# Kernel optimization log

Measured on AMD Instinct MI355X. Metric: run time of the kernel, lower is better.

The kernel has to match this reference:

```python
import jax, jax.numpy as jnp
import numpy as np
from jax import lax

C = 128
HEADS = 8
HID = 256  # int(C * 2.0)
B, H, W = 8, 128, 128
EPS_LN = 1e-5
EPS_NORM = 1e-12


def _dwconv(x, w, pad):
    # x: [B,C,H,W], w: [C,1,kh,kw] depthwise
    return lax.conv_general_dilated(
        x, w, window_strides=(1, 1), padding=[(pad, pad), (pad, pad)],
        dimension_numbers=("NCHW", "OIHW", "NCHW"), feature_group_count=x.shape[1])


def _conv1x1(x, w):
    # w: [O, I] pointwise conv
    return jnp.einsum("oi,bihw->bohw", w, x)


def _layernorm_c(x, gamma, beta):
    # torch: reshape to [B, HW, C], LayerNorm over C, reshape back == LN over channel axis
    mu = jnp.mean(x, axis=1, keepdims=True)
    var = jnp.mean(jnp.square(x - mu), axis=1, keepdims=True)
    xn = (x - mu) * lax.rsqrt(var + EPS_LN)
    return xn * gamma[None, :, None, None] + beta[None, :, None, None]


def _l2norm(x):
    n = jnp.sqrt(jnp.sum(jnp.square(x), axis=-1, keepdims=True))
    return x / jnp.maximum(n, EPS_NORM)


def _mdta(x, qkv_w, qkv_dw, temperature, attn_proj):
    b, c, h, w = x.shape
    qkv = _dwconv(_conv1x1(x, qkv_w), qkv_dw, pad=1)  # [B,3C,H,W]
    q, k, v = jnp.split(qkv, 3, axis=1)
    hd = c // HEADS
    q = q.reshape(b, HEADS, hd, h * w)
    k = k.reshape(b, HEADS, hd, h * w)
    v = v.reshape(b, HEADS, hd, h * w)
    q, k = _l2norm(q), _l2norm(k)
    attn = jax.nn.softmax(jnp.einsum("bhdn,bhen->bhde", q, k) * temperature, axis=-1)
    out = jnp.einsum("bhde,bhen->bhdn", attn, v).reshape(b, c, h, w)
    return _conv1x1(out, attn_proj)


def _gdfn2(x, pin_w, c1_w, c3_w, c5_w, pout_w):
    x = _conv1x1(x, pin_w)  # [B,HID,H,W]
    x1 = x * c1_w[None, :, 0, 0, 0, None, None]  # depthwise 1x1 == per-channel scale
    x3 = _dwconv(x, c3_w, pad=1)
    x5 = _dwconv(x, c5_w, pad=2)
    g = jax.nn.gelu(x1, approximate=False)
    gated = jnp.concatenate([g * x3, g * x5], axis=1)  # [B,2*HID,H,W]
    return _conv1x1(gated, pout_w)


def setup_inputs() -> dict:
    key = jax.random.key(0)
    ks = jax.random.split(key, 12)
    s = 0.05
    return {
        "x": jax.random.normal(ks[0], (B, C, H, W), jnp.float32),
        "ln1_w": jnp.ones((C,), jnp.float32),
        "ln1_b": jnp.zeros((C,), jnp.float32),
        "qkv_w": jax.random.normal(ks[1], (3 * C, C), jnp.float32) * s,
        "qkv_dw": jax.random.normal(ks[2], (3 * C, 1, 3, 3), jnp.float32) * s,
        "temperature": jnp.ones((1, HEADS, 1, 1), jnp.float32),
        "attn_proj": jax.random.normal(ks[3], (C, C), jnp.float32) * s,
        "ln2_w": jnp.ones((C,), jnp.float32),
        "ln2_b": jnp.zeros((C,), jnp.float32),
        "pin_w": jax.random.normal(ks[4], (HID, C), jnp.float32) * s,
        "c1_w": jax.random.normal(ks[5], (HID, 1, 1, 1), jnp.float32) * s,
        "c3_w": jax.random.normal(ks[6], (HID, 1, 3, 3), jnp.float32) * s,
        "c5_w": jax.random.normal(ks[7], (HID, 1, 5, 5), jnp.float32) * s,
        "pout_w": jax.random.normal(ks[8], (C, 2 * HID), jnp.float32) * s,
    }


def reference(x, ln1_w, ln1_b, qkv_w, qkv_dw, temperature, attn_proj,
              ln2_w, ln2_b, pin_w, c1_w, c3_w, c5_w, pout_w):
    x = x + _mdta(_layernorm_c(x, ln1_w, ln1_b), qkv_w, qkv_dw, temperature, attn_proj)
    x = x + _gdfn2(_layernorm_c(x, ln2_w, ln2_b), pin_w, c1_w, c3_w, c5_w, pout_w)
    return x
```

## Files before the change

kernel.cpp:

```cpp
#include <hip/hip_runtime.h>
#include <type_traits>

typedef unsigned short ushort;
typedef unsigned int uint;
typedef __bf16 bf16x8 __attribute__((ext_vector_type(8)));
typedef unsigned short ushort8v __attribute__((ext_vector_type(8)));
typedef float f32x4 __attribute__((ext_vector_type(4)));

__device__ __forceinline__ float b2f(ushort u) {
    unsigned int x = ((unsigned int)u) << 16;
    float f;
    __builtin_memcpy(&f, &x, 4);
    return f;
}
__device__ __forceinline__ ushort f2bf(float f) {
    unsigned int x;
    __builtin_memcpy(&x, &f, 4);
    unsigned int r = x + 0x7fffu + ((x >> 16) & 1u);
    return (ushort)(r >> 16);
}
__device__ __forceinline__ float u2f_lo(uint u) {
    uint x = u << 16;
    float f;
    __builtin_memcpy(&f, &x, 4);
    return f;
}
__device__ __forceinline__ float u2f_hi(uint u) {
    uint x = u & 0xffff0000u;
    float f;
    __builtin_memcpy(&f, &x, 4);
    return f;
}
__device__ __forceinline__ uint packbf(float a, float b) {
    return (uint)f2bf(a) | ((uint)f2bf(b) << 16);
}

#define NPIX 16384
#define PSTRIDE 136

__device__ __forceinline__ size_t tadr(int b, int CH, int tile, int ch, int off) {
    return (((size_t)b * 256 + tile) * CH + ch) * 64 + off;
}
__device__ __forceinline__ size_t padr(int b, int tile, int p, int c) {
    return (((size_t)b * 256 + tile) * 64 + p) * 128 + c;
}

__device__ __forceinline__ void stage_plane(ushort* pl, const ushort* __restrict__ src,
                                            int b, int c, int CH, int tid) {
    uint* plu = (uint*)pl;
    for (int i = tid; i < 784; i += 256) {
        int idx;
        if (i < 136) idx = i;
        else if (i < 272) idx = 8840 + (i - 136);
        else {
            int j = i - 272;
            int r = (j >> 2) + 2;
            int cs = j & 3;
            idx = r * 68 + (cs == 0 ? 0 : 64 + cs);
        }
        plu[idx] = 0u;
    }
    for (int i = tid; i < 2048; i += 256) {
        int row = i >> 4, xg = (i & 15) << 3;
        int px0 = row * 128 + xg;
        uint4 v = *(const uint4*)&src[tadr(b, CH, px0 >> 6, c, px0 & 63)];
        uint* dst = (uint*)&pl[(row + 2) * PSTRIDE + xg + 2];
        dst[0] = v.x; dst[1] = v.y; dst[2] = v.z; dst[3] = v.w;
    }
    __syncthreads();
}

__device__ __forceinline__ void unpack12(const ushort* rowp, float* cc) {
    const uint* rp = (const uint*)rowp;
    uint4 u = *(const uint4*)rp;
    uint2 v = *(const uint2*)(rp + 4);
    cc[0] = u2f_lo(u.x); cc[1] = u2f_hi(u.x);
    cc[2] = u2f_lo(u.y); cc[3] = u2f_hi(u.y);
    cc[4] = u2f_lo(u.z); cc[5] = u2f_hi(u.z);
    cc[6] = u2f_lo(u.w); cc[7] = u2f_hi(u.w);
    cc[8] = u2f_lo(v.x); cc[9] = u2f_hi(v.x);
    cc[10] = u2f_lo(v.y); cc[11] = u2f_hi(v.y);
}

__global__ __launch_bounds__(256) void wcvt(const float* __restrict__ s0, ushort* __restrict__ d0, int n0,
                                            const float* __restrict__ s1, ushort* __restrict__ d1, int n1,
                                            const float* __restrict__ s2, ushort* __restrict__ d2, int n2) {
    int i = blockIdx.x * 256 + threadIdx.x;
    if (i < n0) d0[i] = f2bf(s0[i]);
    else if (i < n0 + n1) d1[i - n0] = f2bf(s1[i - n0]);
    else if (i < n0 + n1 + n2) d2[i - n0 - n1] = f2bf(s2[i - n0 - n1]);
}

template <int O>
__global__ __launch_bounds__(256) void ln_gemm_mfma(const float* __restrict__ xin,
                                                    const ushort* __restrict__ Wb,
                                                    const float* __restrict__ gamma,
                                                    const float* __restrict__ beta,
                                                    ushort* __restrict__ out) {
    __shared__ ushort xs[64][136];
    __shared__ float red[2][4][64];
    __shared__ float mu[64], rs[64];
    __shared__ float gl[128], bl[128];

    const int blk = blockIdx.x;
    const int b = blk >> 8;
    const int tile = blk & 255;
    const int tid = threadIdx.x;

    const float* xb = xin + (size_t)b * 128 * NPIX + tile * 64;
    float vx[4][8];
#pragma unroll
    for (int k = 0; k < 4; k++) {
        int i = tid + k * 256;
        int p = i & 63, cg = i >> 6;
        const float* src = xb + (size_t)(cg * 8) * NPIX + p;
#pragma unroll
        for (int j = 0; j < 8; j++) vx[k][j] = src[(size_t)j * NPIX];
    }
    if (tid < 128) {
        gl[tid] = gamma[tid];
        bl[tid] = beta[tid];
    }
#pragma unroll
    for (int k = 0; k < 4; k++) {
        int i = tid + k * 256;
        int p = i & 63, cg = i >> 6;
        ushort8v u;
#pragma unroll
        for (int j = 0; j < 8; j++) u[j] = f2bf(vx[k][j]);
        *(ushort8v*)&xs[p][cg * 8] = u;
    }
    __syncthreads();

    {
        const int p = tid & 63, part = tid >> 6;
        float s = 0.f, ss = 0.f;
#pragma unroll
        for (int q = 0; q < 4; q++) {
            ushort8v u = *(const ushort8v*)&xs[p][part * 32 + q * 8];
#pragma unroll
            for (int j = 0; j < 8; j++) {
                float v = b2f(u[j]);
                s += v;
                ss += v * v;
            }
        }
        red[0][part][p] = s;
        red[1][part][p] = ss;
    }
    __syncthreads();
    if (tid < 64) {
        float s = red[0][0][tid] + red[0][1][tid] + red[0][2][tid] + red[0][3][tid];
        float ss = red[1][0][tid] + red[1][1][tid] + red[1][2][tid] + red[1][3][tid];
        float m = s * (1.f / 128.f);
        float var = ss * (1.f / 128.f) - m * m;
        mu[tid] = m;
        rs[tid] = rsqrtf(var + 1e-5f);
    }
    __syncthreads();
    {
        const int p = tid & 63, part = tid >> 6;
        const float mp = mu[p], rp = rs[p];
#pragma unroll
        for (int q = 0; q < 4; q++) {
            int c0 = part * 32 + q * 8;
            ushort8v u = *(const ushort8v*)&xs[p][c0];
            ushort8v o;
#pragma unroll
            for (int j = 0; j < 8; j++) {
                float v = b2f(u[j]);
                o[j] = f2bf((v - mp) * rp * gl[c0 + j] + bl[c0 + j]);
            }
            *(ushort8v*)&xs[p][c0] = o;
        }
    }
    __syncthreads();

    const int wv = tid >> 6, lane = tid & 63;
    const int lr = lane & 15, lg = lane >> 4;

    bf16x8 bfr[4][4];
#pragma unroll
    for (int t = 0; t < 4; t++)
#pragma unroll
        for (int kc = 0; kc < 4; kc++)
            bfr[t][kc] = __builtin_bit_cast(bf16x8, *(const ushort8v*)&xs[t * 16 + lr][kc * 32 + lg * 8]);

    constexpr int MT = O / 64;
#pragma unroll 1
    for (int mt = 0; mt < MT; mt++) {
        const int o0 = (wv * MT + mt) * 16;
        bf16x8 afr[4];
#pragma unroll
        for (int kc = 0; kc < 4; kc++)
            afr[kc] = __builtin_bit_cast(bf16x8,
                *(const ushort8v*)&Wb[(size_t)(o0 + lr) * 128 + kc * 32 + lg * 8]);
        f32x4 acc[4] = {{0.f, 0.f, 0.f, 0.f}, {0.f, 0.f, 0.f, 0.f}, {0.f, 0.f, 0.f, 0.f}, {0.f, 0.f, 0.f, 0.f}};
#pragma unroll
        for (int kc = 0; kc < 4; kc++)
#pragma unroll
            for (int t = 0; t < 4; t++)
                acc[t] = __builtin_amdgcn_mfma_f32_16x16x32_bf16(afr[kc], bfr[t][kc], acc[t], 0, 0, 0);
#pragma unroll
        for (int t = 0; t < 4; t++)
#pragma unroll
            for (int r = 0; r < 4; r++) {
                int o = o0 + lg * 4 + r;
                out[tadr(b, O, tile, o, t * 16 + lr)] = f2bf(acc[t][r]);
            }
    }
}

__global__ __launch_bounds__(256) void dwconv3_lds(const ushort* __restrict__ in,
                                                   const float* __restrict__ wdw,
                                                   ushort* __restrict__ out, int CH) {
    __shared__ ushort pl[132 * PSTRIDE];
    const int c = blockIdx.x;
    const int b = blockIdx.y;
    const int tid = threadIdx.x;

    float w[9];
#pragma unroll
    for (int j = 0; j < 9; j++) w[j] = wdw[c * 9 + j];

    stage_plane(pl, in, b, c, CH, tid);

    const int x = (tid & 15) * 8;
    const int ybase = tid >> 4;
#pragma unroll 1
    for (int k = 0; k < 8; k++) {
        const int y = k * 16 + ybase;
        float a[8];
#pragma unroll
        for (int p = 0; p < 8; p++) a[p] = 0.f;
#pragma unroll
        for (int ky = 0; ky < 3; ky++) {
            float cc[12];
            unpack12(&pl[(y + ky + 1) * PSTRIDE + x], cc);
#pragma unroll
            for (int kx = 0; kx < 3; kx++) {
                float wv = w[ky * 3 + kx];
#pragma unroll
                for (int p = 0; p < 8; p++) a[p] += cc[p + kx + 1] * wv;
            }
        }
        const int px0 = (y << 7) + x;
        uint4 o;
        o.x = packbf(a[0], a[1]);
        o.y = packbf(a[2], a[3]);
        o.z = packbf(a[4], a[5]);
        o.w = packbf(a[6], a[7]);
        *(uint4*)&out[tadr(b, CH, px0 >> 6, c, px0 & 63)] = o;
    }
}

__global__ __launch_bounds__(256) void dw_gated(const ushort* __restrict__ t,
                                                const float* __restrict__ w3_,
                                                const float* __restrict__ w5_,
                                                const float* __restrict__ c1w,
                                                ushort* __restrict__ gated) {
    __shared__ ushort pl[132 * PSTRIDE];
    const int c = blockIdx.x;
    const int b = blockIdx.y;
    const int tid = threadIdx.x;

    float w3[9], w5[25];
#pragma unroll
    for (int j = 0; j < 9; j++) w3[j] = w3_[c * 9 + j];
#pragma unroll
    for (int j = 0; j < 25; j++) w5[j] = w5_[c * 25 + j];
    const float c1v = c1w[c];

    stage_plane(pl, t, b, c, 256, tid);

    const int x = (tid & 15) * 8;
    const int ybase = tid >> 4;
#pragma unroll 1
    for (int k = 0; k < 8; k++) {
        const int y = k * 16 + ybase;
        float a5[8], a3[8], tc[8];
#pragma unroll
        for (int p = 0; p < 8; p++) { a5[p] = 0.f; a3[p] = 0.f; }
#pragma unroll
        for (int ky = 0; ky < 5; ky++) {
            float cc[12];
            unpack12(&pl[(y + ky) * PSTRIDE + x], cc);
#pragma unroll
            for (int kx = 0; kx < 5; kx++) {
                float wv = w5[ky * 5 + kx];
#pragma unroll
                for (int p = 0; p < 8; p++) a5[p] += cc[p + kx] * wv;
            }
            if (ky >= 1 && ky <= 3) {
#pragma unroll
                for (int kx = 0; kx < 3; kx++) {
                    float wv = w3[(ky - 1) * 3 + kx];
#pragma unroll
                    for (int p = 0; p < 8; p++) a3[p] += cc[p + kx + 1] * wv;
                }
            }
            if (ky == 2) {
#pragma unroll
                for (int p = 0; p < 8; p++) tc[p] = cc[p + 2];
            }
        }
        const int px0 = (y << 7) + x;
        uint4 o3, o5;
        float g[8];
#pragma unroll
        for (int p = 0; p < 8; p++) {
            float x1 = tc[p] * c1v;
            g[p] = x1 * __builtin_amdgcn_rcpf(1.f + __expf(-1.702f * x1));
        }
        o3.x = packbf(g[0] * a3[0], g[1] * a3[1]);
        o3.y = packbf(g[2] * a3[2], g[3] * a3[3]);
        o3.z = packbf(g[4] * a3[4], g[5] * a3[5]);
        o3.w = packbf(g[6] * a3[6], g[7] * a3[7]);
        o5.x = packbf(g[0] * a5[0], g[1] * a5[1]);
        o5.y = packbf(g[2] * a5[2], g[3] * a5[3]);
        o5.z = packbf(g[4] * a5[4], g[5] * a5[5]);
        o5.w = packbf(g[6] * a5[6], g[7] * a5[7]);
        *(uint4*)&gated[tadr(b, 512, px0 >> 6, c, px0 & 63)] = o3;
        *(uint4*)&gated[tadr(b, 512, px0 >> 6, 256 + c, px0 & 63)] = o5;
    }
}

__global__ __launch_bounds__(256) void attn_M(const ushort* __restrict__ qkv,
                                              const float* __restrict__ temp,
                                              const float* __restrict__ attn_proj,
                                              ushort* __restrict__ M) {
    __shared__ float Sp[4][16][16];
    __shared__ float QSS[4][16], KSS[4][16];
    __shared__ float A[16][17];

    const int bh = blockIdx.x, b = bh >> 3, h = bh & 7;
    const int tid = threadIdx.x;
    const int w = tid >> 6, lane = tid & 63;
    const int lr = lane & 15, lg = lane >> 4;

    const size_t qbase = (((size_t)b * 256 + w * 64) * 384 + h * 16 + lr) * 64 + lg * 8;
    const size_t kbase = qbase + (size_t)128 * 64;

    f32x4 acc = {0.f, 0.f, 0.f, 0.f};
    f32x4 accq = {0.f, 0.f, 0.f, 0.f};
    f32x4 acck = {0.f, 0.f, 0.f, 0.f};
#pragma unroll 2
    for (int it = 0; it < 128; it++) {
        size_t off = (size_t)(it >> 1) * (384 * 64) + (it & 1) * 32;
        bf16x8 qf = __builtin_bit_cast(bf16x8, *(const ushort8v*)(qkv + qbase + off));
        bf16x8 kf = __builtin_bit_cast(bf16x8, *(const ushort8v*)(qkv + kbase + off));
        acc = __builtin_amdgcn_mfma_f32_16x16x32_bf16(qf, kf, acc, 0, 0, 0);
        accq = __builtin_amdgcn_mfma_f32_16x16x32_bf16(qf, qf, accq, 0, 0, 0);
        acck = __builtin_amdgcn_mfma_f32_16x16x32_bf16(kf, kf, acck, 0, 0, 0);
    }
#pragma unroll
    for (int r = 0; r < 4; r++) Sp[w][lg * 4 + r][lr] = acc[r];
    if (lg == (lr >> 2)) {
        QSS[w][lr] = accq[lr & 3];
        KSS[w][lr] = acck[lr & 3];
    }
    __syncthreads();

    const int d = tid >> 4, e = tid & 15;
    float S = Sp[0][d][e] + Sp[1][d][e] + Sp[2][d][e] + Sp[3][d][e];
    float nq = fmaxf(sqrtf(QSS[0][d] + QSS[1][d] + QSS[2][d] + QSS[3][d]), 1e-12f);
    float nk = fmaxf(sqrtf(KSS[0][e] + KSS[1][e] + KSS[2][e] + KSS[3][e]), 1e-12f);
    float logit = S / (nq * nk) * temp[h];
    float m = logit;
    for (int off = 8; off; off >>= 1) m = fmaxf(m, __shfl_xor(m, off, 64));
    float ex = expf(logit - m);
    float sum = ex;
    for (int off = 8; off; off >>= 1) sum += __shfl_xor(sum, off, 64);
    A[d][e] = ex / sum;
    __syncthreads();

    for (int i = tid; i < 2048; i += 256) {
        int o = i >> 4, ee = i & 15;
        float acc2 = 0.f;
#pragma unroll
        for (int dd = 0; dd < 16; dd++) acc2 += attn_proj[o * 128 + h * 16 + dd] * A[dd][ee];
        M[((size_t)b * 128 + o) * 128 + h * 16 + ee] = f2bf(acc2);
    }
}

__global__ __launch_bounds__(256) void mv_ln_mfma(const ushort* __restrict__ qkv,
                                                  const ushort* __restrict__ Mb16,
                                                  const float* __restrict__ x,
                                                  const ushort* __restrict__ pin_b,
                                                  const float* __restrict__ gamma,
                                                  const float* __restrict__ beta,
                                                  ushort* __restrict__ x2,
                                                  ushort* __restrict__ t_out) {
    __shared__ ushort vs[64][136];
    __shared__ ushort xs[64][136];
    __shared__ float red[2][4][64];
    __shared__ float mu[64], rs[64];
    __shared__ float gl[128], bl[128];

    const int blk = blockIdx.x;
    const int b = blk >> 8;
    const int tile = blk & 255;
    const int tid = threadIdx.x;
    const int wv = tid >> 6, lane = tid & 63;
    const int lr = lane & 15, lg = lane >> 4;

    const ushort* vb = qkv + tadr(b, 384, tile, 256, 0);
    ushort8v vv[4];
#pragma unroll
    for (int k = 0; k < 4; k++) {
        int idx = tid + k * 256;
        int c = idx & 127, pg = idx >> 7;
        vv[k] = *(const ushort8v*)&vb[c * 64 + pg * 8];
    }
    if (tid < 128) {
        gl[tid] = gamma[tid];
        bl[tid] = beta[tid];
    }
#pragma unroll
    for (int k = 0; k < 4; k++) {
        int idx = tid + k * 256;
        int c = idx & 127, pg = idx >> 7;
#pragma unroll
        for (int j = 0; j < 8; j++) vs[pg * 8 + j][c] = vv[k][j];
    }
    __syncthreads();

    bf16x8 bfr[4][4];
#pragma unroll
    for (int t = 0; t < 4; t++)
#pragma unroll
        for (int kc = 0; kc < 4; kc++)
            bfr[t][kc] = __builtin_bit_cast(bf16x8, *(const ushort8v*)&vs[t * 16 + lr][kc * 32 + lg * 8]);

    const ushort* Mb = Mb16 + (size_t)b * 128 * 128;
#pragma unroll 1
    for (int mt = 0; mt < 2; mt++) {
        const int o0 = (wv * 2 + mt) * 16;
        bf16x8 afr[4];
#pragma unroll
        for (int kc = 0; kc < 4; kc++)
            afr[kc] = __builtin_bit_cast(bf16x8,
                *(const ushort8v*)&Mb[(size_t)(o0 + lr) * 128 + kc * 32 + lg * 8]);
        f32x4 acc[4] = {{0.f, 0.f, 0.f, 0.f}, {0.f, 0.f, 0.f, 0.f}, {0.f, 0.f, 0.f, 0.f}, {0.f, 0.f, 0.f, 0.f}};
#pragma unroll
        for (int kc = 0; kc < 4; kc++)
#pragma unroll
            for (int t = 0; t < 4; t++)
                acc[t] = __builtin_amdgcn_mfma_f32_16x16x32_bf16(afr[kc], bfr[t][kc], acc[t], 0, 0, 0);
#pragma unroll
        for (int t = 0; t < 4; t++) {
            int px = t * 16 + lr;
            const float* xp = &x[((size_t)b * 128 + o0 + lg * 4) * NPIX + tile * 64 + px];
            uint2 pk;
            pk.x = packbf(xp[0] + acc[t][0], xp[NPIX] + acc[t][1]);
            pk.y = packbf(xp[2 * NPIX] + acc[t][2], xp[3 * NPIX] + acc[t][3]);
            *(uint2*)&xs[px][o0 + lg * 4] = pk;
        }
    }
    __syncthreads();

#pragma unroll
    for (int k = 0; k < 4; k++) {
        int idx = tid + k * 256;
        int p = idx >> 4, seg = idx & 15;
        uint4 v = *(const uint4*)&xs[p][seg * 8];
        *(uint4*)&x2[padr(b, tile, p, seg * 8)] = v;
    }
    {
        const int p = tid & 63, part = tid >> 6;
        float s = 0.f, ss = 0.f;
#pragma unroll
        for (int q = 0; q < 4; q++) {
            ushort8v u = *(const ushort8v*)&xs[p][part * 32 + q * 8];
#pragma unroll
            for (int j = 0; j < 8; j++) {
                float v = b2f(u[j]);
                s += v;
                ss += v * v;
            }
        }
        red[0][part][p] = s;
        red[1][part][p] = ss;
    }
    __syncthreads();
    if (tid < 64) {
        float s = red[0][0][tid] + red[0][1][tid] + red[0][2][tid] + red[0][3][tid];
        float ss = red[1][0][tid] + red[1][1][tid] + red[1][2][tid] + red[1][3][tid];
        float m = s * (1.f / 128.f);
        float var = ss * (1.f / 128.f) - m * m;
        mu[tid] = m;
        rs[tid] = rsqrtf(var + 1e-5f);
    }
    __syncthreads();
    {
        const int p = tid & 63, part = tid >> 6;
        const float mp = mu[p], rp = rs[p];
#pragma unroll
        for (int q = 0; q < 4; q++) {
            int c0 = part * 32 + q * 8;
            ushort8v u = *(const ushort8v*)&xs[p][c0];
            ushort8v o;
#pragma unroll
            for (int j = 0; j < 8; j++) {
                float v = b2f(u[j]);
                o[j] = f2bf((v - mp) * rp * gl[c0 + j] + bl[c0 + j]);
            }
            *(ushort8v*)&xs[p][c0] = o;
        }
    }
    __syncthreads();

    bf16x8 bfr2[4][4];
#pragma unroll
    for (int t = 0; t < 4; t++)
#pragma unroll
        for (int kc = 0; kc < 4; kc++)
            bfr2[t][kc] = __builtin_bit_cast(bf16x8, *(const ushort8v*)&xs[t * 16 + lr][kc * 32 + lg * 8]);

#pragma unroll 1
    for (int mt = 0; mt < 4; mt++) {
        const int o0 = (wv * 4 + mt) * 16;
        bf16x8 afr[4];
#pragma unroll
        for (int kc = 0; kc < 4; kc++)
            afr[kc] = __builtin_bit_cast(bf16x8,
                *(const ushort8v*)&pin_b[(size_t)(o0 + lr) * 128 + kc * 32 + lg * 8]);
        f32x4 acc[4] = {{0.f, 0.f, 0.f, 0.f}, {0.f, 0.f, 0.f, 0.f}, {0.f, 0.f, 0.f, 0.f}, {0.f, 0.f, 0.f, 0.f}};
#pragma unroll
        for (int kc = 0; kc < 4; kc++)
#pragma unroll
            for (int t = 0; t < 4; t++)
                acc[t] = __builtin_amdgcn_mfma_f32_16x16x32_bf16(afr[kc], bfr2[t][kc], acc[t], 0, 0, 0);
#pragma unroll
        for (int t = 0; t < 4; t++)
#pragma unroll
            for (int r = 0; r < 4; r++) {
                int o = o0 + lg * 4 + r;
                t_out[tadr(b, 256, tile, o, t * 16 + lr)] = f2bf(acc[t][r]);
            }
    }
}

__global__ __launch_bounds__(256) void gdfn_mfma(const ushort* __restrict__ gated,
                                                 const ushort* __restrict__ x2,
                                                 const ushort* __restrict__ pout_b,
                                                 float* __restrict__ out) {
    __shared__ ushort gs[2][64][72];

    const int blk = blockIdx.x;
    const int b = blk >> 8;
    const int tile = blk & 255;
    const int tid = threadIdx.x;
    const int wv = tid >> 6, lane = tid & 63;
    const int lr = lane & 15, lg = lane >> 4;

    const ushort* gb = gated + tadr(b, 512, tile, 0, 0);
    const int c0 = tid & 63;
    const int pg0 = tid >> 6;

    ushort8v pa[8], pb[8];
#pragma unroll
    for (int k = 0; k < 8; k++) {
        const ushort* nb = gb + k * 4096;
        pa[k] = *(const ushort8v*)&nb[c0 * 64 + pg0 * 8];
        pb[k] = *(const ushort8v*)&nb[c0 * 64 + (pg0 + 4) * 8];
    }

    f32x4 acc[2][4];
#pragma unroll
    for (int mt = 0; mt < 2; mt++)
#pragma unroll
        for (int tt = 0; tt < 4; tt++) acc[mt][tt] = (f32x4){0.f, 0.f, 0.f, 0.f};

#pragma unroll
    for (int j = 0; j < 8; j++) {
        gs[0][pg0 * 8 + j][c0] = pa[0][j];
        gs[0][(pg0 + 4) * 8 + j][c0] = pb[0][j];
    }
    __syncthreads();

#pragma unroll
    for (int kb = 0; kb < 8; kb++) {
        const int cur = kb & 1;

        bf16x8 bfrg[4][2];
#pragma unroll
        for (int tt = 0; tt < 4; tt++)
#pragma unroll
            for (int kc = 0; kc < 2; kc++)
                bfrg[tt][kc] = __builtin_bit_cast(bf16x8, *(const ushort8v*)&gs[cur][tt * 16 + lr][kc * 32 + lg * 8]);

#pragma unroll
        for (int mt = 0; mt < 2; mt++) {
            const int o0 = (wv * 2 + mt) * 16;
            bf16x8 afr[2];
#pragma unroll
            for (int kc = 0; kc < 2; kc++)
                afr[kc] = __builtin_bit_cast(bf16x8,
                    *(const ushort8v*)&pout_b[(size_t)(o0 + lr) * 512 + kb * 64 + kc * 32 + lg * 8]);
#pragma unroll
            for (int kc = 0; kc < 2; kc++)
#pragma unroll
                for (int tt = 0; tt < 4; tt++)
                    acc[mt][tt] = __builtin_amdgcn_mfma_f32_16x16x32_bf16(afr[kc], bfrg[tt][kc], acc[mt][tt], 0, 0, 0);
        }

        if (kb < 7) {
#pragma unroll
            for (int j = 0; j < 8; j++) {
                gs[cur ^ 1][pg0 * 8 + j][c0] = pa[kb + 1][j];
                gs[cur ^ 1][(pg0 + 4) * 8 + j][c0] = pb[kb + 1][j];
            }
        }
        __syncthreads();
    }

#pragma unroll
    for (int mt = 0; mt < 2; mt++)
#pragma unroll
        for (int tt = 0; tt < 4; tt++) {
            int o0 = (wv * 2 + mt) * 16 + lg * 4;
            int px = tt * 16 + lr;
            uint2 xw = *(const uint2*)&x2[padr(b, tile, px, o0)];
            float xv0 = u2f_lo(xw.x), xv1 = u2f_hi(xw.x);
            float xv2 = u2f_lo(xw.y), xv3 = u2f_hi(xw.y);
            size_t obase = ((size_t)b * 128 + o0) * NPIX + tile * 64 + px;
            out[obase] = xv0 + acc[mt][tt][0];
            out[obase + NPIX] = xv1 + acc[mt][tt][1];
            out[obase + 2 * NPIX] = xv2 + acc[mt][tt][2];
            out[obase + 3 * NPIX] = xv3 + acc[mt][tt][3];
        }
}

extern "C" void kernel_launch(void* const* d_in, const int* in_sizes, int n_in,
                              void* d_out, int out_size, void* d_ws, size_t ws_size,
                              hipStream_t stream) {
    const float* x = (const float*)d_in[0];
    const float* ln1_w = (const float*)d_in[1];
    const float* ln1_b = (const float*)d_in[2];
    const float* qkv_w = (const float*)d_in[3];
    const float* qkv_dw = (const float*)d_in[4];
    const float* temperature = (const float*)d_in[5];
    const float* attn_proj = (const float*)d_in[6];
    const float* ln2_w = (const float*)d_in[7];
    const float* ln2_b = (const float*)d_in[8];
    const float* pin_w = (const float*)d_in[9];
    const float* c1_w = (const float*)d_in[10];
    const float* c3_w = (const float*)d_in[11];
    const float* c5_w = (const float*)d_in[12];
    const float* pout_w = (const float*)d_in[13];
    float* out = (float*)d_out;

    char* ws = (char*)d_ws;
    ushort* qkv_pre = (ushort*)(ws + 0);
    ushort* qkv     = (ushort*)(ws + 100663296);
    ushort* x2      = (ushort*)(ws + 201326592);
    ushort* t       = (ushort*)(ws + 0);
    ushort* gated   = (ushort*)(ws + 67108864);
    ushort* Mb16    = (ushort*)(ws + 235151360);
    ushort* qkv_wb  = (ushort*)(ws + 235413504);
    ushort* pin_wb  = (ushort*)(ws + 235511808);
    ushort* pout_wb = (ushort*)(ws + 235577344);

    wcvt<<<576, 256, 0, stream>>>(qkv_w, qkv_wb, 49152, pin_w, pin_wb, 32768, pout_w, pout_wb, 65536);
    ln_gemm_mfma<384><<<2048, 256, 0, stream>>>(x, qkv_wb, ln1_w, ln1_b, qkv_pre);
    dwconv3_lds<<<dim3(384, 8), 256, 0, stream>>>(qkv_pre, qkv_dw, qkv, 384);
    attn_M<<<64, 256, 0, stream>>>(qkv, temperature, attn_proj, Mb16);
    mv_ln_mfma<<<2048, 256, 0, stream>>>(qkv, Mb16, x, pin_wb, ln2_w, ln2_b, x2, t);
    dw_gated<<<dim3(256, 8), 256, 0, stream>>>(t, c3_w, c5_w, c1_w, gated);
    gdfn_mfma<<<2048, 256, 0, stream>>>(gated, x2, pout_wb, out);
}
```

Measured before the change: 317.7 us.

## Prefetch MFMA weight fragments and restream gated tiles per k-block

The 1x1-conv MFMA loops now prefetch the next output tile's weight fragments into a double buffer and are fully unrolled. The attention-output kernel loads all M fragments up front, before the V staging. In gdfn_mfma, the gated tile is no longer preloaded whole into 16 vector registers. Each k-block is instead fetched with scalar 16-bit loads, one iteration ahead, and written to LDS as 8-wide vector stores in a transposed layout. The aim is to hide global-load latency and cut register pressure, at the cost of many narrow uncoalesced-looking 2-byte loads and more live registers in the unrolled loops.

```diff
diff --git a/kernel.cpp b/kernel.cpp
--- a/kernel.cpp
+++ b/kernel.cpp
@@ -187,20 +187,30 @@
             bfr[t][kc] = __builtin_bit_cast(bf16x8, *(const ushort8v*)&xs[t * 16 + lr][kc * 32 + lg * 8]);
 
     constexpr int MT = O / 64;
-#pragma unroll 1
+    bf16x8 afp[2][4];
+    {
+        const int o0 = (wv * MT) * 16;
+#pragma unroll
+        for (int kc = 0; kc < 4; kc++)
+            afp[0][kc] = __builtin_bit_cast(bf16x8,
+                *(const ushort8v*)&Wb[(size_t)(o0 + lr) * 128 + kc * 32 + lg * 8]);
+    }
+#pragma unroll
     for (int mt = 0; mt < MT; mt++) {
+        if (mt + 1 < MT) {
+            const int o0n = (wv * MT + mt + 1) * 16;
+#pragma unroll
+            for (int kc = 0; kc < 4; kc++)
+                afp[(mt + 1) & 1][kc] = __builtin_bit_cast(bf16x8,
+                    *(const ushort8v*)&Wb[(size_t)(o0n + lr) * 128 + kc * 32 + lg * 8]);
+        }
         const int o0 = (wv * MT + mt) * 16;
-        bf16x8 afr[4];
+        f32x4 acc[4] = {{0.f, 0.f, 0.f, 0.f}, {0.f, 0.f, 0.f, 0.f}, {0.f, 0.f, 0.f, 0.f}, {0.f, 0.f, 0.f, 0.f}};
 #pragma unroll
         for (int kc = 0; kc < 4; kc++)
-            afr[kc] = __builtin_bit_cast(bf16x8,
-                *(const ushort8v*)&Wb[(size_t)(o0 + lr) * 128 + kc * 32 + lg * 8]);
-        f32x4 acc[4] = {{0.f, 0.f, 0.f, 0.f}, {0.f, 0.f, 0.f, 0.f}, {0.f, 0.f, 0.f, 0.f}, {0.f, 0.f, 0.f, 0.f}};
-#pragma unroll
-        for (int kc = 0; kc < 4; kc++)
 #pragma unroll
             for (int t = 0; t < 4; t++)
-                acc[t] = __builtin_amdgcn_mfma_f32_16x16x32_bf16(afr[kc], bfr[t][kc], acc[t], 0, 0, 0);
+                acc[t] = __builtin_amdgcn_mfma_f32_16x16x32_bf16(afp[mt & 1][kc], bfr[t][kc], acc[t], 0, 0, 0);
 #pragma unroll
         for (int t = 0; t < 4; t++)
 #pragma unroll
@@ -404,6 +414,15 @@
     const int wv = tid >> 6, lane = tid & 63;
     const int lr = lane & 15, lg = lane >> 4;
 
+    const ushort* Mb = Mb16 + (size_t)b * 128 * 128;
+    bf16x8 mfr[2][4];
+#pragma unroll
+    for (int mt = 0; mt < 2; mt++)
+#pragma unroll
+        for (int kc = 0; kc < 4; kc++)
+            mfr[mt][kc] = __builtin_bit_cast(bf16x8,
+                *(const ushort8v*)&Mb[(size_t)((wv * 2 + mt) * 16 + lr) * 128 + kc * 32 + lg * 8]);
+
     const ushort* vb = qkv + tadr(b, 384, tile, 256, 0);
     ushort8v vv[4];
 #pragma unroll
@@ -432,21 +451,15 @@
         for (int kc = 0; kc < 4; kc++)
             bfr[t][kc] = __builtin_bit_cast(bf16x8, *(const ushort8v*)&vs[t * 16 + lr][kc * 32 + lg * 8]);
 
-    const ushort* Mb = Mb16 + (size_t)b * 128 * 128;
-#pragma unroll 1
+#pragma unroll
     for (int mt = 0; mt < 2; mt++) {
         const int o0 = (wv * 2 + mt) * 16;
-        bf16x8 afr[4];
+        f32x4 acc[4] = {{0.f, 0.f, 0.f, 0.f}, {0.f, 0.f, 0.f, 0.f}, {0.f, 0.f, 0.f, 0.f}, {0.f, 0.f, 0.f, 0.f}};
 #pragma unroll
         for (int kc = 0; kc < 4; kc++)
-            afr[kc] = __builtin_bit_cast(bf16x8,
-                *(const ushort8v*)&Mb[(size_t)(o0 + lr) * 128 + kc * 32 + lg * 8]);
-        f32x4 acc[4] = {{0.f, 0.f, 0.f, 0.f}, {0.f, 0.f, 0.f, 0.f}, {0.f, 0.f, 0.f, 0.f}, {0.f, 0.f, 0.f, 0.f}};
-#pragma unroll
-        for (int kc = 0; kc < 4; kc++)
 #pragma unroll
             for (int t = 0; t < 4; t++)
-                acc[t] = __builtin_amdgcn_mfma_f32_16x16x32_bf16(afr[kc], bfr[t][kc], acc[t], 0, 0, 0);
+                acc[t] = __builtin_amdgcn_mfma_f32_16x16x32_bf16(mfr[mt][kc], bfr[t][kc], acc[t], 0, 0, 0);
 #pragma unroll
         for (int t = 0; t < 4; t++) {
             int px = t * 16 + lr;
@@ -457,6 +470,12 @@
             *(uint2*)&xs[px][o0 + lg * 4] = pk;
         }
     }
+
+    bf16x8 pfp[2][4];
+#pragma unroll
+    for (int kc = 0; kc < 4; kc++)
+        pfp[0][kc] = __builtin_bit_cast(bf16x8,
+            *(const ushort8v*)&pin_b[(size_t)((wv * 4) * 16 + lr) * 128 + kc * 32 + lg * 8]);
     __syncthreads();
 
 #pragma unroll
@@ -517,20 +536,22 @@
         for (int kc = 0; kc < 4; kc++)
             bfr2[t][kc] = __builtin_bit_cast(bf16x8, *(const ushort8v*)&xs[t * 16 + lr][kc * 32 + lg * 8]);
 
-#pragma unroll 1
+#pragma unroll
     for (int mt = 0; mt < 4; mt++) {
+        if (mt + 1 < 4) {
+            const int o0n = (wv * 4 + mt + 1) * 16;
+#pragma unroll
+            for (int kc = 0; kc < 4; kc++)
+                pfp[(mt + 1) & 1][kc] = __builtin_bit_cast(bf16x8,
+                    *(const ushort8v*)&pin_b[(size_t)(o0n + lr) * 128 + kc * 32 + lg * 8]);
+        }
         const int o0 = (wv * 4 + mt) * 16;
-        bf16x8 afr[4];
+        f32x4 acc[4] = {{0.f, 0.f, 0.f, 0.f}, {0.f, 0.f, 0.f, 0.f}, {0.f, 0.f, 0.f, 0.f}, {0.f, 0.f, 0.f, 0.f}};
 #pragma unroll
         for (int kc = 0; kc < 4; kc++)
-            afr[kc] = __builtin_bit_cast(bf16x8,
-                *(const ushort8v*)&pin_b[(size_t)(o0 + lr) * 128 + kc * 32 + lg * 8]);
-        f32x4 acc[4] = {{0.f, 0.f, 0.f, 0.f}, {0.f, 0.f, 0.f, 0.f}, {0.f, 0.f, 0.f, 0.f}, {0.f, 0.f, 0.f, 0.f}};
-#pragma unroll
-        for (int kc = 0; kc < 4; kc++)
 #pragma unroll
             for (int t = 0; t < 4; t++)
-                acc[t] = __builtin_amdgcn_mfma_f32_16x16x32_bf16(afr[kc], bfr2[t][kc], acc[t], 0, 0, 0);
+                acc[t] = __builtin_amdgcn_mfma_f32_16x16x32_bf16(pfp[mt & 1][kc], bfr2[t][kc], acc[t], 0, 0, 0);
 #pragma unroll
         for (int t = 0; t < 4; t++)
 #pragma unroll
@@ -555,16 +576,8 @@
     const int lr = lane & 15, lg = lane >> 4;
 
     const ushort* gb = gated + tadr(b, 512, tile, 0, 0);
-    const int c0 = tid & 63;
-    const int pg0 = tid >> 6;
-
-    ushort8v pa[8], pb[8];
-#pragma unroll
-    for (int k = 0; k < 8; k++) {
-        const ushort* nb = gb + k * 4096;
-        pa[k] = *(const ushort8v*)&nb[c0 * 64 + pg0 * 8];
-        pb[k] = *(const ushort8v*)&nb[c0 * 64 + (pg0 + 4) * 8];
-    }
+    const int p0 = tid & 63;
+    const int kga = tid >> 6;
 
     f32x4 acc[2][4];
 #pragma unroll
@@ -572,16 +585,32 @@
 #pragma unroll
         for (int tt = 0; tt < 4; tt++) acc[mt][tt] = (f32x4){0.f, 0.f, 0.f, 0.f};
 
-#pragma unroll
-    for (int j = 0; j < 8; j++) {
-        gs[0][pg0 * 8 + j][c0] = pa[0][j];
-        gs[0][(pg0 + 4) * 8 + j][c0] = pb[0][j];
+    {
+        ushort ca[8], cb[8];
+#pragma unroll
+        for (int j = 0; j < 8; j++) ca[j] = gb[(kga * 8 + j) * 64 + p0];
+#pragma unroll
+        for (int j = 0; j < 8; j++) cb[j] = gb[((kga + 4) * 8 + j) * 64 + p0];
+        ushort8v ua, ub;
+#pragma unroll
+        for (int j = 0; j < 8; j++) { ua[j] = ca[j]; ub[j] = cb[j]; }
+        *(ushort8v*)&gs[0][p0][kga * 8] = ua;
+        *(ushort8v*)&gs[0][p0][(kga + 4) * 8] = ub;
     }
     __syncthreads();
 
 #pragma unroll
     for (int kb = 0; kb < 8; kb++) {
         const int cur = kb & 1;
+
+        ushort na[8], nb[8];
+        if (kb < 7) {
+            const ushort* nbp = gb + (kb + 1) * 4096;
+#pragma unroll
+            for (int j = 0; j < 8; j++) na[j] = nbp[(kga * 8 + j) * 64 + p0];
+#pragma unroll
+            for (int j = 0; j < 8; j++) nb[j] = nbp[((kga + 4) * 8 + j) * 64 + p0];
+        }
 
         bf16x8 bfrg[4][2];
 #pragma unroll
@@ -606,11 +635,11 @@
         }
 
         if (kb < 7) {
-#pragma unroll
-            for (int j = 0; j < 8; j++) {
-                gs[cur ^ 1][pg0 * 8 + j][c0] = pa[kb + 1][j];
-                gs[cur ^ 1][(pg0 + 4) * 8 + j][c0] = pb[kb + 1][j];
-            }
+            ushort8v ua, ub;
+#pragma unroll
+            for (int j = 0; j < 8; j++) { ua[j] = na[j]; ub[j] = nb[j]; }
+            *(ushort8v*)&gs[cur ^ 1][p0][kga * 8] = ua;
+            *(ushort8v*)&gs[cur ^ 1][p0][(kga + 4) * 8] = ub;
         }
         __syncthreads();
     }
```

Measured after the change: 312.9 us. Within noise of the previous version (-1.5%).
